# Optimization experiments

Hardware: AMD Instinct MI355X
Metric: run time of the kernel (lower is better)

## Reference

```python
import jax, jax.numpy as jnp
import numpy as np

B, T, D, H, E, M = 4, 2048, 2048, 8, 512, 8  # batch, seq, hidden, moe_heads, moe_experts, moe_dim//2
F = E * M  # flatten_shape = 4096
HALF = D // 2


def act(z):
    # 'relu2' activation: relu(x)**2
    r = jax.nn.relu(z)
    return r * r


def setup_inputs() -> dict:
    key = jax.random.key(0)
    ks = jax.random.split(key, 13)
    s = 0.02
    return {
        "x": jax.random.normal(ks[0], (B, T, D), jnp.float32),
        "g1": jax.random.uniform(ks[1], (B, T, H, E), jnp.float32),
        "g2": jax.random.uniform(ks[2], (B, T, H, E), jnp.float32),
        "u1_w": jax.random.normal(ks[3], (F, D), jnp.float32) * s,
        "u1_b": jnp.zeros((F,), jnp.float32),
        "u2_w": jax.random.normal(ks[4], (F, D), jnp.float32) * s,
        "u2_b": jnp.zeros((F,), jnp.float32),
        "v11_w": jax.random.normal(ks[5], (HALF, F), jnp.float32) * s,
        "v12_w": jax.random.normal(ks[6], (HALF, F), jnp.float32) * s,
        "v21_w": jax.random.normal(ks[7], (HALF, F), jnp.float32) * s,
        "v22_w": jax.random.normal(ks[8], (HALF, F), jnp.float32) * s,
        "b1": jax.random.normal(ks[9], (E, HALF), jnp.float32) * s,
        "b2": jax.random.normal(ks[10], (E, HALF), jnp.float32) * s,
    }


def reference(x, g1, g2, u1_w, u1_b, u2_w, u2_b, v11_w, v12_w, v21_w, v22_w, b1, b2):
    # x1, x2: [B,T,E,M]
    x1 = act(x @ u1_w.T + u1_b).reshape(B, T, E, M)
    x2 = act(x @ u2_w.T + u2_b).reshape(B, T, E, M)

    g1s = g1.sum(axis=2)  # [B,T,E] (einsum '...hi->...i')
    g2s = g2.sum(axis=2)

    # x11 = v11(einsum('btim,bthi->btim', x1, g1).flatten(-2))
    x11 = (x1 * g1s[..., None]).reshape(B, T, F) @ v11_w.T
    # x12 = v12(einsum('btjm,bthj,bthi->btim', x2, g2, g1).flatten(-2))
    t2 = jnp.einsum('btjm,bthj->bthm', x2, g2)
    x12 = jnp.einsum('bthm,bthi->btim', t2, g1).reshape(B, T, F) @ v12_w.T
    # x13 = einsum('bthi,id->btd', g1, b1)
    x13 = g1s @ b1

    # x21 = v21(einsum('btim,bthi,bthj->btjm', x1, g1, g2).flatten(-2))
    t1 = jnp.einsum('btim,bthi->bthm', x1, g1)
    x21 = jnp.einsum('bthm,bthj->btjm', t1, g2).reshape(B, T, F) @ v21_w.T
    # x22 = v22(einsum('btjm,bthj->btjm', x2, g2).flatten(-2))
    x22 = (x2 * g2s[..., None]).reshape(B, T, F) @ v22_w.T
    # x23 = einsum('bthj,jd->btd', g2, b2)
    x23 = g2s @ b2

    return jnp.concatenate((x11 + x12 + x13, x21 + x22 + x23), axis=-1)
```

## Files before the change

### kernel.cpp

```cpp
#include <hip/hip_runtime.h>
#include <hip/hip_bf16.h>

#define TOK   8192
#define DD    2048
#define FF    4096
#define EE    512
#define HALF  1024
#define KCAT  8704

typedef __bf16 bf16x8 __attribute__((ext_vector_type(8)));
typedef __bf16 bf16x4 __attribute__((ext_vector_type(4)));
typedef float  f32x4  __attribute__((ext_vector_type(4)));
using bf16 = __hip_bfloat16;

#define AS1(p) ((const __attribute__((address_space(1))) void*)(p))
#define AS3(p) ((__attribute__((address_space(3))) void*)(p))

#define PR0 4194304u
#define PR1 6291456u
#define PR2 8388608u
#define PR3 10485760u
#define PR4 12582912u
#define PR5 13631488u
__global__ __launch_bounds__(256)
void prep_all(const float* __restrict__ x, const float* __restrict__ u1_w,
              const float* __restrict__ u2_w,
              const float* __restrict__ v11, const float* __restrict__ v12,
              const float* __restrict__ v21, const float* __restrict__ v22,
              const float* __restrict__ b1, const float* __restrict__ b2,
              bf16* __restrict__ Xb, bf16* __restrict__ U1b, bf16* __restrict__ U2b,
              bf16* __restrict__ Wl, bf16* __restrict__ Wr)
{
    const unsigned stride = gridDim.x * blockDim.x;
    for (unsigned i = blockIdx.x * blockDim.x + threadIdx.x; i < PR5; i += stride) {
        if (i < PR2) {
            const float* src; bf16* dst; unsigned s;
            if (i < PR0)      { s = i;        src = x;    dst = Xb;  }
            else if (i < PR1) { s = i - PR0;  src = u1_w; dst = U1b; }
            else              { s = i - PR1;  src = u2_w; dst = U2b; }
            float4 v = ((const float4*)src)[s];
            bf16x4 o;
            o[0] = (__bf16)v.x; o[1] = (__bf16)v.y; o[2] = (__bf16)v.z; o[3] = (__bf16)v.w;
            ((bf16x4*)dst)[s] = o;
        } else if (i < PR4) {
            const bool left = (i < PR3);
            unsigned s = i - (left ? PR2 : PR3);
            unsigned n = s >> 11, j = s & 2047;
            const float* vs = left ? (j < 1024 ? v11 : v12) : (j < 1024 ? v21 : v22);
            unsigned jj = (j < 1024) ? j : (j - 1024);
            float4 v = *(const float4*)(vs + (size_t)n * FF + jj * 4);
            bf16x4 o;
            o[0] = (__bf16)v.x; o[1] = (__bf16)v.y; o[2] = (__bf16)v.z; o[3] = (__bf16)v.w;
            bf16* wb = left ? Wl : Wr;
            *(bf16x4*)(wb + (size_t)n * KCAT + ((j < 1024) ? 0 : FF) + jj * 4) = o;
        } else {
            unsigned s = i - PR4;
            const bool left = (s < (unsigned)(HALF * EE));
            unsigned r = left ? s : s - HALF * EE;
            unsigned n = r >> 9, e = r & 511;
            const float* bm = left ? b1 : b2;
            bf16* wb = left ? Wl : Wr;
            wb[(size_t)n * KCAT + 2 * FF + e] = __float2bfloat16(bm[(size_t)e * HALF + n]);
        }
    }
}

template<int MODE>
__global__ __launch_bounds__(512, 2)
void gemmP(const bf16* __restrict__ A0, const bf16* __restrict__ B0,
           const float* __restrict__ bias0, void* __restrict__ C0,
           const bf16* __restrict__ A1, const bf16* __restrict__ B1,
           const float* __restrict__ bias1, void* __restrict__ C1,
           int nbm, int nbn, int K, int ldc)
{
    __shared__ __align__(16) char smem[131072];
    const int tid  = threadIdx.x;
    const int lane = tid & 63;
    const int wid  = tid >> 6;
    const int wm = wid >> 2, wn = wid & 3;
    const int r16 = lane & 15, kb = lane >> 4;

    int bid = blockIdx.x;
    {
        int nwg = gridDim.x;
        int q = nwg >> 3, r = nwg & 7;
        int xcd = bid & 7, idx = bid >> 3;
        bid = (xcd < r ? xcd * (q + 1) : r * (q + 1) + (xcd - r) * q) + idx;
    }
    const int npg = nbm * nbn;
    const int g   = bid / npg;
    const int lb  = bid - g * npg;
    const int bm = lb / nbn, bn = lb - bm * nbn;

    const bf16*  A    = g ? A1 : A0;
    const bf16*  Bw   = g ? B1 : B0;
    const float* bias = g ? bias1 : bias0;
    char* Cout = (char*)(g ? C1 : C0);

    const long row0 = (long)bm * 256;
    const int  col0 = bn * 256;
    const int  nt   = K >> 6;

    const char* gA[2]; const char* gB[2];
    #pragma unroll
    for (int l = 0; l < 2; ++l) {
        const uint32_t S = (uint32_t)(l * 512 + tid) * 16;
        const int r  = (int)(S >> 6);
        const int cb = (int)((S & 63) ^ ((uint32_t)((r >> 1) & 3) << 4));
        gA[l] = (const char*)A  + (row0 + r) * (long)K * 2 + cb;
        gB[l] = (const char*)Bw + (long)(col0 + r) * K * 2 + cb;
    }
    const uint32_t ldst = (uint32_t)(tid & ~63) * 16;

    const uint32_t swz  = ((uint32_t)(r16 >> 1) & 3u) << 4;
    const uint32_t aoff = (uint32_t)((wm * 128 + r16) * 64 + kb * 16) ^ swz;
    const uint32_t boff = (uint32_t)((wn * 64  + r16) * 64 + kb * 16) ^ swz;

    f32x4 acc[8][4];
    #pragma unroll
    for (int i = 0; i < 8; ++i)
        #pragma unroll
        for (int j = 0; j < 4; ++j)
            acc[i][j] = (f32x4){0.f, 0.f, 0.f, 0.f};

    __builtin_amdgcn_global_load_lds(AS1(gA[0]),      AS3(smem +     0 + ldst), 16, 0, 0);
    __builtin_amdgcn_global_load_lds(AS1(gA[1]),      AS3(smem +  8192 + ldst), 16, 0, 0);
    __builtin_amdgcn_global_load_lds(AS1(gB[0]),      AS3(smem + 32768 + ldst), 16, 0, 0);
    __builtin_amdgcn_global_load_lds(AS1(gB[1]),      AS3(smem + 40960 + ldst), 16, 0, 0);
    __builtin_amdgcn_global_load_lds(AS1(gA[0] + 64), AS3(smem + 16384 + ldst), 16, 0, 0);
    __builtin_amdgcn_global_load_lds(AS1(gA[1] + 64), AS3(smem + 24576 + ldst), 16, 0, 0);
    __builtin_amdgcn_global_load_lds(AS1(gB[0] + 64), AS3(smem + 49152 + ldst), 16, 0, 0);
    __builtin_amdgcn_global_load_lds(AS1(gB[1] + 64), AS3(smem + 57344 + ldst), 16, 0, 0);
    asm volatile("s_waitcnt vmcnt(4)\n\ts_barrier" ::: "memory");

    bf16x8 afA[4], afB[4], bv0[4], bv1[4];
    #pragma unroll
    for (int f = 0; f < 4; ++f) {
        afA[f] = *(const bf16x8*)(smem +     0 + aoff + f * 1024);
        bv0[f] = *(const bf16x8*)(smem + 32768 + boff + f * 1024);
    }

#define MFMA16(AF, BV, IH)                                                              \
    __builtin_amdgcn_s_setprio(1);                                                      \
    _Pragma("unroll")                                                                   \
    for (int fi = 0; fi < 4; ++fi) {                                                    \
        acc[(IH)*4+fi][0] = __builtin_amdgcn_mfma_f32_16x16x32_bf16(AF[fi], BV[0], acc[(IH)*4+fi][0], 0, 0, 0); \
        acc[(IH)*4+fi][1] = __builtin_amdgcn_mfma_f32_16x16x32_bf16(AF[fi], BV[1], acc[(IH)*4+fi][1], 0, 0, 0); \
        acc[(IH)*4+fi][2] = __builtin_amdgcn_mfma_f32_16x16x32_bf16(AF[fi], BV[2], acc[(IH)*4+fi][2], 0, 0, 0); \
        acc[(IH)*4+fi][3] = __builtin_amdgcn_mfma_f32_16x16x32_bf16(AF[fi], BV[3], acc[(IH)*4+fi][3], 0, 0, 0); \
    }                                                                                   \
    __builtin_amdgcn_s_setprio(0);

    for (int t = 0; t < nt; ++t) {
        const char* pb = smem + (t & 1) * 65536;
        char*       pt = smem + ((t + 1) & 1) * 65536;
        const bool  st = (t + 1 < nt);
        const long  koff = (long)(t + 1) * 128;

        if (st) {
            __builtin_amdgcn_global_load_lds(AS1(gA[0] + koff), AS3(pt +    0 + ldst), 16, 0, 0);
            __builtin_amdgcn_global_load_lds(AS1(gA[1] + koff), AS3(pt + 8192 + ldst), 16, 0, 0);
        }
        asm volatile("s_barrier" ::: "memory");
        #pragma unroll
        for (int f = 0; f < 4; ++f)
            afB[f] = *(const bf16x8*)(pb + 4096 + aoff + f * 1024);
        MFMA16(afA, bv0, 0)

        if (st) {
            __builtin_amdgcn_global_load_lds(AS1(gB[0] + koff), AS3(pt + 32768 + ldst), 16, 0, 0);
            __builtin_amdgcn_global_load_lds(AS1(gB[1] + koff), AS3(pt + 40960 + ldst), 16, 0, 0);
            asm volatile("s_waitcnt vmcnt(4)" ::: "memory");
        } else {
            asm volatile("s_waitcnt vmcnt(0)" ::: "memory");
        }
        asm volatile("s_barrier" ::: "memory");
        #pragma unroll
        for (int f = 0; f < 4; ++f) {
            afA[f] = *(const bf16x8*)(pb + 16384 + aoff + f * 1024);
            bv1[f] = *(const bf16x8*)(pb + 49152 + boff + f * 1024);
        }
        MFMA16(afB, bv0, 1)

        if (st) {
            __builtin_amdgcn_global_load_lds(AS1(gA[0] + koff + 64), AS3(pt + 16384 + ldst), 16, 0, 0);
            __builtin_amdgcn_global_load_lds(AS1(gA[1] + koff + 64), AS3(pt + 24576 + ldst), 16, 0, 0);
        }
        asm volatile("s_barrier" ::: "memory");
        #pragma unroll
        for (int f = 0; f < 4; ++f)
            afB[f] = *(const bf16x8*)(pb + 16384 + 4096 + aoff + f * 1024);
        MFMA16(afA, bv1, 0)

        if (st) {
            __builtin_amdgcn_global_load_lds(AS1(gB[0] + koff + 64), AS3(pt + 49152 + ldst), 16, 0, 0);
            __builtin_amdgcn_global_load_lds(AS1(gB[1] + koff + 64), AS3(pt + 57344 + ldst), 16, 0, 0);
            asm volatile("s_waitcnt vmcnt(4)" ::: "memory");
        }
        asm volatile("s_barrier" ::: "memory");
        if (st) {
            #pragma unroll
            for (int f = 0; f < 4; ++f) {
                afA[f] = *(const bf16x8*)(pt +     0 + aoff + f * 1024);
                bv0[f] = *(const bf16x8*)(pt + 32768 + boff + f * 1024);
            }
        }
        MFMA16(afB, bv1, 1)
    }
#undef MFMA16

    const int rb = (lane >> 4) * 4;
    #pragma unroll
    for (int i = 0; i < 8; ++i) {
        #pragma unroll
        for (int j = 0; j < 4; ++j) {
            const int cc = col0 + wn * 64 + j * 16 + r16;
            float badd = 0.f;
            if (MODE == 1) badd = bias[cc];
            #pragma unroll
            for (int e = 0; e < 4; ++e) {
                long row = row0 + wm * 128 + i * 16 + rb + e;
                float v = acc[i][j][e];
                if (MODE == 1) {
                    v += badd;
                    v = fmaxf(v, 0.f);
                    v = v * v;
                    ((bf16*)Cout)[row * ldc + cc] = __float2bfloat16(v);
                } else {
                    ((float*)Cout)[row * ldc + cc] = v;
                }
            }
        }
    }
}

#define GPAD 524
__global__ __launch_bounds__(256)
void glue(const float* __restrict__ g1, const float* __restrict__ g2,
          bf16* __restrict__ Yl, bf16* __restrict__ Yr)
{
    __shared__ __align__(16) float g1t[8 * GPAD];
    __shared__ __align__(16) float g2t[8 * GPAD];
    __shared__ float g1s[EE], g2s[EE];
    __shared__ float t1s[64], t2s[64];
    __shared__ float t1p[4][64], t2p[4][64];
    __shared__ __align__(16) bf16 x1t[FF], x2t[FF];

    const int t   = blockIdx.x;
    const int tid = threadIdx.x;
    const float* g1p = g1 + (size_t)t * FF;
    const float* g2p = g2 + (size_t)t * FF;
    bf16* ylp = Yl + (size_t)t * KCAT;
    bf16* yrp = Yr + (size_t)t * KCAT;

    #pragma unroll
    for (int c = 0; c < 4; ++c) {
        int idx4 = (c * 256 + tid) * 4;
        float4 v1 = *(const float4*)(g1p + idx4);
        float4 v2 = *(const float4*)(g2p + idx4);
        int h = idx4 >> 9, e = idx4 & 511;
        *(float4*)&g1t[h * GPAD + e] = v1;
        *(float4*)&g2t[h * GPAD + e] = v2;
    }
    #pragma unroll
    for (int c = 0; c < 2; ++c) {
        int idx8 = (c * 256 + tid) * 8;
        *(bf16x8*)&x1t[idx8] = *(const bf16x8*)(ylp + idx8);
        *(bf16x8*)&x2t[idx8] = *(const bf16x8*)(yrp + FF + idx8);
    }
    __syncthreads();

    #pragma unroll
    for (int c = 0; c < 2; ++c) {
        int e = c * 256 + tid;
        float s1 = 0.f, s2 = 0.f;
        #pragma unroll
        for (int h = 0; h < 8; ++h) { s1 += g1t[h * GPAD + e]; s2 += g2t[h * GPAD + e]; }
        g1s[e] = s1; g2s[e] = s2;
    }

    {
        int o = tid & 63;
        int h = o & 7, m = o >> 3;
        int p = tid >> 6;
        float s1 = 0.f, s2 = 0.f;
        #pragma unroll 8
        for (int ii = 0; ii < 128; ++ii) {
            int e = p * 128 + ii;
            float xv1 = __bfloat162float(x1t[e * 8 + m]);
            float xv2 = __bfloat162float(x2t[e * 8 + m]);
            s1 += xv1 * g1t[h * GPAD + e];
            s2 += xv2 * g2t[h * GPAD + e];
        }
        t1p[p][o] = s1; t2p[p][o] = s2;
    }
    __syncthreads();
    if (tid < 64)       t1s[tid] = t1p[0][tid] + t1p[1][tid] + t1p[2][tid] + t1p[3][tid];
    else if (tid < 128) { int o = tid - 64; t2s[o] = t2p[0][o] + t2p[1][o] + t2p[2][o] + t2p[3][o]; }
    __syncthreads();

    #pragma unroll
    for (int c = 0; c < 2; ++c) {
        int f0 = (c * 256 + tid) * 8;
        int e  = f0 >> 3;
        float s1 = g1s[e], s2 = g2s[e];
        bf16x8 xa = *(const bf16x8*)&x1t[f0];
        bf16x8 xb = *(const bf16x8*)&x2t[f0];
        bf16x8 o1, o2;
        #pragma unroll
        for (int u = 0; u < 8; ++u) {
            o1[u] = (__bf16)((float)xa[u] * s1);
            o2[u] = (__bf16)((float)xb[u] * s2);
        }
        *(bf16x8*)(ylp + f0)      = o1;
        *(bf16x8*)(yrp + FF + f0) = o2;
    }
    #pragma unroll
    for (int c = 0; c < 2; ++c) {
        int f0 = (c * 256 + tid) * 8;
        int i  = f0 >> 3;
        bf16x8 o12v, o21v;
        #pragma unroll
        for (int m = 0; m < 8; ++m) {
            float s12 = 0.f, s21 = 0.f;
            #pragma unroll
            for (int h = 0; h < 8; ++h) {
                s12 += t2s[(m << 3) | h] * g1t[h * GPAD + i];
                s21 += t1s[(m << 3) | h] * g2t[h * GPAD + i];
            }
            o12v[m] = (__bf16)s12;
            o21v[m] = (__bf16)s21;
        }
        *(bf16x8*)(ylp + FF + f0) = o12v;
        *(bf16x8*)(yrp + f0)      = o21v;
    }
    {
        int e0 = tid * 2;
        ylp[2 * FF + e0]     = __float2bfloat16(g1s[e0]);
        ylp[2 * FF + e0 + 1] = __float2bfloat16(g1s[e0 + 1]);
        yrp[2 * FF + e0]     = __float2bfloat16(g2s[e0]);
        yrp[2 * FF + e0 + 1] = __float2bfloat16(g2s[e0 + 1]);
    }
}


extern "C" void kernel_launch(void* const* d_in, const int* in_sizes, int n_in,
                              void* d_out, int out_size, void* d_ws, size_t ws_size,
                              hipStream_t stream) {
    const float* x    = (const float*)d_in[0];
    const float* g1   = (const float*)d_in[1];
    const float* g2   = (const float*)d_in[2];
    const float* u1_w = (const float*)d_in[3];
    const float* u1_b = (const float*)d_in[4];
    const float* u2_w = (const float*)d_in[5];
    const float* u2_b = (const float*)d_in[6];
    const float* v11  = (const float*)d_in[7];
    const float* v12  = (const float*)d_in[8];
    const float* v21  = (const float*)d_in[9];
    const float* v22  = (const float*)d_in[10];
    const float* b1   = (const float*)d_in[11];
    const float* b2   = (const float*)d_in[12];
    float* out = (float*)d_out;

    size_t off = 0;
    char* base = (char*)d_ws;
    auto take = [&](size_t bytes) { void* p = base + off; off += (bytes + 255) & ~(size_t)255; return p; };
    bf16* Xb  = (bf16*)take((size_t)TOK * DD * 2);
    bf16* U1b = (bf16*)take((size_t)FF * DD * 2);
    bf16* U2b = (bf16*)take((size_t)FF * DD * 2);
    bf16* Wl  = (bf16*)take((size_t)HALF * KCAT * 2);
    bf16* Wr  = (bf16*)take((size_t)HALF * KCAT * 2);
    bf16* Yl  = (bf16*)take((size_t)TOK * KCAT * 2);
    bf16* Yr  = (bf16*)take((size_t)TOK * KCAT * 2);

    prep_all<<<2048, 256, 0, stream>>>(x, u1_w, u2_w, v11, v12, v21, v22, b1, b2,
                                       Xb, U1b, U2b, Wl, Wr);

    gemmP<1><<<2 * (TOK / 256) * (FF / 256), 512, 0, stream>>>(
        Xb, U1b, u1_b, Yl,
        Xb, U2b, u2_b, Yr + FF,
        TOK / 256, FF / 256, DD, KCAT);

    glue<<<TOK, 256, 0, stream>>>(g1, g2, Yl, Yr);

    gemmP<0><<<2 * (TOK / 256) * (HALF / 256), 512, 0, stream>>>(
        Yl, Wl, nullptr, out,
        Yr, Wr, nullptr, out + HALF,
        TOK / 256, HALF / 256, KCAT, DD);
}
```

Before: 685.0 us.

## Move second-stage weight conversion into extra blocks of the first GEMM

Result: no change. 684.1 us (-0.1%).

```diff
diff --git a/kernel.cpp b/kernel.cpp
--- a/kernel.cpp
+++ b/kernel.cpp
@@ -19,49 +19,21 @@
 #define PR0 4194304u
 #define PR1 6291456u
 #define PR2 8388608u
-#define PR3 10485760u
-#define PR4 12582912u
-#define PR5 13631488u
 __global__ __launch_bounds__(256)
-void prep_all(const float* __restrict__ x, const float* __restrict__ u1_w,
+void prep_cvt(const float* __restrict__ x, const float* __restrict__ u1_w,
               const float* __restrict__ u2_w,
-              const float* __restrict__ v11, const float* __restrict__ v12,
-              const float* __restrict__ v21, const float* __restrict__ v22,
-              const float* __restrict__ b1, const float* __restrict__ b2,
-              bf16* __restrict__ Xb, bf16* __restrict__ U1b, bf16* __restrict__ U2b,
-              bf16* __restrict__ Wl, bf16* __restrict__ Wr)
+              bf16* __restrict__ Xb, bf16* __restrict__ U1b, bf16* __restrict__ U2b)
 {
     const unsigned stride = gridDim.x * blockDim.x;
-    for (unsigned i = blockIdx.x * blockDim.x + threadIdx.x; i < PR5; i += stride) {
-        if (i < PR2) {
-            const float* src; bf16* dst; unsigned s;
-            if (i < PR0)      { s = i;        src = x;    dst = Xb;  }
-            else if (i < PR1) { s = i - PR0;  src = u1_w; dst = U1b; }
-            else              { s = i - PR1;  src = u2_w; dst = U2b; }
-            float4 v = ((const float4*)src)[s];
-            bf16x4 o;
-            o[0] = (__bf16)v.x; o[1] = (__bf16)v.y; o[2] = (__bf16)v.z; o[3] = (__bf16)v.w;
-            ((bf16x4*)dst)[s] = o;
-        } else if (i < PR4) {
-            const bool left = (i < PR3);
-            unsigned s = i - (left ? PR2 : PR3);
-            unsigned n = s >> 11, j = s & 2047;
-            const float* vs = left ? (j < 1024 ? v11 : v12) : (j < 1024 ? v21 : v22);
-            unsigned jj = (j < 1024) ? j : (j - 1024);
-            float4 v = *(const float4*)(vs + (size_t)n * FF + jj * 4);
-            bf16x4 o;
-            o[0] = (__bf16)v.x; o[1] = (__bf16)v.y; o[2] = (__bf16)v.z; o[3] = (__bf16)v.w;
-            bf16* wb = left ? Wl : Wr;
-            *(bf16x4*)(wb + (size_t)n * KCAT + ((j < 1024) ? 0 : FF) + jj * 4) = o;
-        } else {
-            unsigned s = i - PR4;
-            const bool left = (s < (unsigned)(HALF * EE));
-            unsigned r = left ? s : s - HALF * EE;
-            unsigned n = r >> 9, e = r & 511;
-            const float* bm = left ? b1 : b2;
-            bf16* wb = left ? Wl : Wr;
-            wb[(size_t)n * KCAT + 2 * FF + e] = __float2bfloat16(bm[(size_t)e * HALF + n]);
-        }
+    for (unsigned i = blockIdx.x * blockDim.x + threadIdx.x; i < PR2; i += stride) {
+        const float* src; bf16* dst; unsigned s;
+        if (i < PR0)      { s = i;        src = x;    dst = Xb;  }
+        else if (i < PR1) { s = i - PR0;  src = u1_w; dst = U1b; }
+        else              { s = i - PR1;  src = u2_w; dst = U2b; }
+        float4 v = ((const float4*)src)[s];
+        bf16x4 o;
+        o[0] = (__bf16)v.x; o[1] = (__bf16)v.y; o[2] = (__bf16)v.z; o[3] = (__bf16)v.w;
+        ((bf16x4*)dst)[s] = o;
     }
 }
 
@@ -71,10 +43,45 @@
            const float* __restrict__ bias0, void* __restrict__ C0,
            const bf16* __restrict__ A1, const bf16* __restrict__ B1,
            const float* __restrict__ bias1, void* __restrict__ C1,
-           int nbm, int nbn, int K, int ldc)
+           int nbm, int nbn, int K, int ldc,
+           const float* __restrict__ xv11, const float* __restrict__ xv12,
+           const float* __restrict__ xv21, const float* __restrict__ xv22,
+           const float* __restrict__ xb1, const float* __restrict__ xb2,
+           bf16* __restrict__ xWl, bf16* __restrict__ xWr)
 {
     __shared__ __align__(16) char smem[131072];
     const int tid  = threadIdx.x;
+    const int npg  = nbm * nbn;
+
+    if (MODE == 1 && blockIdx.x >= (unsigned)(2 * npg)) {
+        const unsigned lane_g = (blockIdx.x - 2 * npg) * 512u + tid;
+        #pragma unroll 4
+        for (int k = 0; k < 32; ++k) {
+            unsigned w = lane_g + (unsigned)k * 131072u;
+            const bool left = w < 2097152u;
+            unsigned s = left ? w : w - 2097152u;
+            unsigned n = s >> 11, j = s & 2047u;
+            const float* vs = left ? (j < 1024u ? xv11 : xv12) : (j < 1024u ? xv21 : xv22);
+            unsigned jj = (j < 1024u) ? j : (j - 1024u);
+            float4 v = *(const float4*)(vs + (size_t)n * FF + jj * 4);
+            bf16x4 o;
+            o[0] = (__bf16)v.x; o[1] = (__bf16)v.y; o[2] = (__bf16)v.z; o[3] = (__bf16)v.w;
+            bf16* wb = left ? xWl : xWr;
+            *(bf16x4*)(wb + (size_t)n * KCAT + ((j < 1024u) ? 0 : FF) + jj * 4) = o;
+        }
+        #pragma unroll 2
+        for (int k = 0; k < 8; ++k) {
+            unsigned w = lane_g + (unsigned)k * 131072u;
+            const bool left = w < 524288u;
+            unsigned r = left ? w : w - 524288u;
+            unsigned n = r >> 9, e = r & 511u;
+            const float* bm = left ? xb1 : xb2;
+            bf16* wb = left ? xWl : xWr;
+            wb[(size_t)n * KCAT + 2 * FF + e] = __float2bfloat16(bm[(size_t)e * HALF + n]);
+        }
+        return;
+    }
+
     const int lane = tid & 63;
     const int wid  = tid >> 6;
     const int wm = wid >> 2, wn = wid & 3;
@@ -82,12 +89,11 @@
 
     int bid = blockIdx.x;
     {
-        int nwg = gridDim.x;
+        int nwg = 2 * npg;
         int q = nwg >> 3, r = nwg & 7;
         int xcd = bid & 7, idx = bid >> 3;
         bid = (xcd < r ? xcd * (q + 1) : r * (q + 1) + (xcd - r) * q) + idx;
     }
-    const int npg = nbm * nbn;
     const int g   = bid / npg;
     const int lb  = bid - g * npg;
     const int bm = lb / nbn, bn = lb - bm * nbn;
@@ -373,18 +379,19 @@
     bf16* Yl  = (bf16*)take((size_t)TOK * KCAT * 2);
     bf16* Yr  = (bf16*)take((size_t)TOK * KCAT * 2);
 
-    prep_all<<<2048, 256, 0, stream>>>(x, u1_w, u2_w, v11, v12, v21, v22, b1, b2,
-                                       Xb, U1b, U2b, Wl, Wr);
-
-    gemmP<1><<<2 * (TOK / 256) * (FF / 256), 512, 0, stream>>>(
+    prep_cvt<<<2048, 256, 0, stream>>>(x, u1_w, u2_w, Xb, U1b, U2b);
+
+    gemmP<1><<<2 * (TOK / 256) * (FF / 256) + 256, 512, 0, stream>>>(
         Xb, U1b, u1_b, Yl,
         Xb, U2b, u2_b, Yr + FF,
-        TOK / 256, FF / 256, DD, KCAT);
+        TOK / 256, FF / 256, DD, KCAT,
+        v11, v12, v21, v22, b1, b2, Wl, Wr);
 
     glue<<<TOK, 256, 0, stream>>>(g1, g2, Yl, Yr);
 
     gemmP<0><<<2 * (TOK / 256) * (HALF / 256), 512, 0, stream>>>(
         Yl, Wl, nullptr, out,
         Yr, Wr, nullptr, out + HALF,
-        TOK / 256, HALF / 256, KCAT, DD);
+        TOK / 256, HALF / 256, KCAT, DD,
+        nullptr, nullptr, nullptr, nullptr, nullptr, nullptr, nullptr, nullptr);
 }
```
